# Performance work log

Measured on AMD Instinct MI355X. Metric: run time of the kernel, lower is better.

## Reference

```python
import jax, jax.numpy as jnp
import numpy as np

N = 50000      # nodes
E = 800000     # edges per meta-path
P = 3          # meta-paths
IN = 128       # in_size
H = 8          # heads
D = 32         # out_size per head
EMB = 128      # embedding_dim


def setup_inputs() -> dict:
    key = jax.random.key(0)
    ks = jax.random.split(key, 7)
    h = jax.random.normal(ks[0], (N, IN), jnp.float32)
    edge_index = jax.random.randint(ks[1], (P, 2, E), 0, N, dtype=jnp.int32)
    fc_w = jax.random.normal(ks[2], (P, IN, H * D), jnp.float32) * 0.05
    attn_l = jax.random.normal(ks[3], (P, H, D), jnp.float32) * 0.1
    attn_r = jax.random.normal(ks[4], (P, H, D), jnp.float32) * 0.1
    sem_w = jax.random.normal(ks[5], (P * H * D, EMB), jnp.float32) * 0.05
    sem_b = jnp.zeros((EMB,), jnp.float32)
    return {"h": h, "edge_index": edge_index, "fc_w": fc_w,
            "attn_l": attn_l, "attn_r": attn_r, "sem_w": sem_w, "sem_b": sem_b}


def _gat(h, W, al, ar, src, dst):
    # DGL GATConv (no bias/residual), eval mode (no dropout)
    feat = (h @ W).reshape(N, H, D)                      # (N,H,D)
    el = jnp.einsum('nhd,hd->nh', feat, al)              # (N,H)
    er = jnp.einsum('nhd,hd->nh', feat, ar)
    e = jax.nn.leaky_relu(el[src] + er[dst], negative_slope=0.2)  # (E,H)
    # edge softmax over incoming edges of each dst node
    m = jax.ops.segment_max(e, dst, num_segments=N)      # (N,H); -inf only for empty segs (never indexed)
    ex = jnp.exp(e - m[dst])
    den = jax.ops.segment_sum(ex, dst, num_segments=N)   # (N,H)
    a = ex / den[dst]                                    # (E,H)
    msg = feat[src] * a[..., None]                       # (E,H,D) gather + weight
    out = jax.ops.segment_sum(msg, dst, num_segments=N)  # (N,H,D) scatter-add
    return jax.nn.elu(out).reshape(N, H * D)             # flatten(1)


def reference(h, edge_index, fc_w, attn_l, attn_r, sem_w, sem_b):
    src = edge_index[:, 0]  # (P,E)
    dst = edge_index[:, 1]
    # run one GATConv per meta-path, vectorized over the meta-path axis
    z = jax.vmap(_gat, in_axes=(None, 0, 0, 0, 0, 0))(h, fc_w, attn_l, attn_r, src, dst)  # (P,N,H*D)
    z = jnp.transpose(z, (1, 0, 2)).reshape(N, P * H * D)  # stack(dim=1) then reshape [N,-1]
    return z @ sem_w + sem_b                                # SemanticAttention.project2
```

## Files before the change

kernel.cpp:

```cpp
#include <hip/hip_runtime.h>
#include <hip/hip_bf16.h>

#define N_NODES 50000
#define N_EDGES 800000
#define NPATH 3
#define NBKT 196
#define NBKT3 (NPATH * NBKT)
#define NCHUNKBLK 256
#define CHUNK 9375
#define LDS_STRIDE 260

typedef __attribute__((ext_vector_type(8))) short short8;
typedef __attribute__((ext_vector_type(4))) float v4f;

__device__ __forceinline__ short f2bf(float v, float* back) {
  unsigned u = __float_as_uint(v);
  unsigned r = (u + 0x7FFFu + ((u >> 16) & 1u)) >> 16;
  *back = __uint_as_float(r << 16);
  return (short)r;
}

__global__ __launch_bounds__(256) void blk_count_kernel(
    const int* __restrict__ ei, int* __restrict__ cntmat) {
  __shared__ int lcnt[NBKT3];
  const int t = threadIdx.x, blk = blockIdx.x;
  for (int j = t; j < NBKT3; j += 256) lcnt[j] = 0;
  __syncthreads();
  const int lo = blk * CHUNK, hi = lo + CHUNK;
  for (int idx = lo + t; idx < hi; idx += 256) {
    int p = idx / N_EDGES, e = idx - p * N_EDGES;
    int d = ei[p * 2 * N_EDGES + N_EDGES + e];
    atomicAdd(&lcnt[p * NBKT + (d >> 8)], 1);
  }
  __syncthreads();
  for (int j = t; j < NBKT3; j += 256) cntmat[blk * NBKT3 + j] = lcnt[j];
}

__global__ __launch_bounds__(256) void col_scan_kernel(
    const int* __restrict__ cntmat, int* __restrict__ pos, int* __restrict__ btot) {
  __shared__ int tmp[256];
  const int b = blockIdx.x, t = threadIdx.x;
  int v = cntmat[t * NBKT3 + b];
  tmp[t] = v;
  __syncthreads();
  for (int ofs = 1; ofs < 256; ofs <<= 1) {
    int x = (t >= ofs) ? tmp[t - ofs] : 0;
    __syncthreads();
    tmp[t] += x;
    __syncthreads();
  }
  pos[b * 256 + t] = tmp[t] - v;
  if (t == 255) btot[b] = tmp[255];
}

__global__ __launch_bounds__(1024) void bucket_scan_kernel(
    const int* __restrict__ btot, int* __restrict__ boff) {
  __shared__ int tmp[1024];
  const int t = threadIdx.x;
  int v = (t < NBKT3) ? btot[t] : 0;
  tmp[t] = v;
  __syncthreads();
  for (int ofs = 1; ofs < 1024; ofs <<= 1) {
    int x = (t >= ofs) ? tmp[t - ofs] : 0;
    __syncthreads();
    tmp[t] += x;
    __syncthreads();
  }
  if (t < NBKT3) boff[t] = tmp[t] - v;
}

__global__ __launch_bounds__(256) void scatter_det_kernel(
    const int* __restrict__ ei, const int* __restrict__ boff,
    const int* __restrict__ pos, int2* __restrict__ ebuf) {
  __shared__ int cursor[NBKT3];
  const int t = threadIdx.x, blk = blockIdx.x;
  for (int j = t; j < NBKT3; j += 256)
    cursor[j] = boff[j] + pos[j * 256 + blk];
  __syncthreads();
  const int lo = blk * CHUNK, hi = lo + CHUNK;
  for (int idx = lo + t; idx < hi; idx += 256) {
    int p = idx / N_EDGES, e = idx - p * N_EDGES;
    int s = ei[p * 2 * N_EDGES + e];
    int d = ei[p * 2 * N_EDGES + N_EDGES + e];
    int ps = atomicAdd(&cursor[p * NBKT + (d >> 8)], 1);
    ebuf[ps] = make_int2(s, d);
  }
}

__global__ __launch_bounds__(256) void bucket_csr_kernel(
    const int2* __restrict__ ebuf, const int* __restrict__ boff,
    const int* __restrict__ btot,
    int* __restrict__ off3, int* __restrict__ deg3, int* __restrict__ csr_src) {
  __shared__ int cnt[256], excl[256], cur[256];
  const int b = blockIdx.x;
  const int t = threadIdx.x;
  const int p = b / NBKT;
  const int node_base = (b - p * NBKT) * 256;
  const int start = boff[b];
  const int ecount = btot[b];

  cnt[t] = 0;
  __syncthreads();
  for (int i = t; i < ecount; i += 256)
    atomicAdd(&cnt[ebuf[start + i].y & 255], 1);
  __syncthreads();

  int v = cnt[t];
  excl[t] = v;
  __syncthreads();
  for (int ofs = 1; ofs < 256; ofs <<= 1) {
    int x = (t >= ofs) ? excl[t - ofs] : 0;
    __syncthreads();
    excl[t] += x;
    __syncthreads();
  }
  int my_excl = excl[t] - v;
  cur[t] = my_excl;
  const int node = node_base + t;
  if (node < N_NODES) {
    off3[p * N_NODES + node] = start + my_excl;
    deg3[p * N_NODES + node] = v;
  }
  __syncthreads();

  for (int i = t; i < ecount; i += 256) {
    int2 e = ebuf[start + i];
    int pos2 = atomicAdd(&cur[e.y & 255], 1);
    csr_src[start + pos2] = e.x;
  }
}

__global__ __launch_bounds__(256) void prep_kernel(
    const float* __restrict__ fc_w, const float* __restrict__ attn_l,
    const float* __restrict__ attn_r, const float* __restrict__ sem_w,
    __hip_bfloat16* __restrict__ Wf_hi, __hip_bfloat16* __restrict__ Wf_lo,
    __hip_bfloat16* __restrict__ Bs_hi, __hip_bfloat16* __restrict__ Bs_lo) {
  const int p = blockIdx.x / 33;
  const int unit = blockIdx.x % 33;
  const int t = threadIdx.x;
  if (unit < 17) {
    const float* W = fc_w + (size_t)p * 128 * 256;
    int idx = unit * 256 + t;
    int lane = idx & 63;
    int tmp = idx >> 6;
    int nt = tmp % 17, kc = tmp / 17;
    int l15 = lane & 15, quad = lane >> 4;
    __hip_bfloat16* oh = Wf_hi + (size_t)p * 34816;
    __hip_bfloat16* ol = Wf_lo + (size_t)p * 34816;
    for (int j = 0; j < 8; j++) {
      int k = kc * 32 + quad * 8 + j;
      float v;
      if (nt < 16) {
        v = W[k * 256 + nt * 16 + l15];
      } else {
        int h8 = l15 & 7;
        const float* av = ((l15 < 8) ? attn_l : attn_r) + (size_t)p * 256 + h8 * 32;
        v = 0.f;
        for (int dd = 0; dd < 32; dd++)
          v = fmaf(W[k * 256 + h8 * 32 + dd], av[dd], v);
      }
      float back, back2;
      short hb = f2bf(v, &back);
      short lb = f2bf(v - back, &back2);
      ((short*)oh)[(tmp * 64 + lane) * 8 + j] = hb;
      ((short*)ol)[(tmp * 64 + lane) * 8 + j] = lb;
    }
  } else {
    const float* Ws = sem_w + (size_t)p * 256 * 128;
    int idx = (unit - 17) * 256 + t;
    int lane = idx & 63;
    int tmp = idx >> 6;
    int nt = tmp & 7, kc = tmp >> 3;
    int l15 = lane & 15, quad = lane >> 4;
    __hip_bfloat16* oh = Bs_hi + (size_t)p * 32768;
    __hip_bfloat16* ol = Bs_lo + (size_t)p * 32768;
    for (int j = 0; j < 8; j++) {
      int k = kc * 32 + quad * 8 + j;
      float v = Ws[k * 128 + nt * 16 + l15];
      float back, back2;
      short hb = f2bf(v, &back);
      short lb = f2bf(v - back, &back2);
      ((short*)oh)[(tmp * 64 + lane) * 8 + j] = hb;
      ((short*)ol)[(tmp * 64 + lane) * 8 + j] = lb;
    }
  }
}

__global__ __launch_bounds__(64) void feat_mfma_kernel(
    const float* __restrict__ h,
    const __hip_bfloat16* __restrict__ Wf_hi_all,
    const __hip_bfloat16* __restrict__ Wf_lo_all,
    __hip_bfloat16* __restrict__ feat3, float* __restrict__ el3,
    float* __restrict__ er3) {
  const int p = blockIdx.y;
  const __hip_bfloat16* Wf_hi = Wf_hi_all + (size_t)p * 34816;
  const __hip_bfloat16* Wf_lo = Wf_lo_all + (size_t)p * 34816;
  __hip_bfloat16* feat = feat3 + (size_t)p * N_NODES * 256;
  float* el = el3 + (size_t)p * N_NODES * 8;
  float* er = er3 + (size_t)p * N_NODES * 8;

  const int lane = threadIdx.x;
  const int l15 = lane & 15, quad = lane >> 4;
  const int m0 = blockIdx.x * 16;
  const int mrow = m0 + l15;

  v4f acc[17];
#pragma unroll
  for (int nt = 0; nt < 17; nt++) acc[nt] = {0.f, 0.f, 0.f, 0.f};

#pragma unroll
  for (int kc = 0; kc < 4; kc++) {
    const float* hrow = h + (size_t)mrow * 128 + kc * 32 + quad * 8;
    float4 fa = *(const float4*)hrow;
    float4 fb = *(const float4*)(hrow + 4);
    float fv[8] = {fa.x, fa.y, fa.z, fa.w, fb.x, fb.y, fb.z, fb.w};
    short8 ahi, alo;
#pragma unroll
    for (int q = 0; q < 8; q++) {
      float back, back2;
      ahi[q] = f2bf(fv[q], &back);
      alo[q] = f2bf(fv[q] - back, &back2);
    }
#pragma unroll
    for (int nt = 0; nt < 17; nt++) {
      const int o = ((kc * 17 + nt) * 64 + lane) * 8;
      short8 bhi = *(const short8*)(Wf_hi + o);
      short8 blo = *(const short8*)(Wf_lo + o);
      acc[nt] = __builtin_amdgcn_mfma_f32_16x16x32_bf16(ahi, bhi, acc[nt], 0, 0, 0);
      acc[nt] = __builtin_amdgcn_mfma_f32_16x16x32_bf16(ahi, blo, acc[nt], 0, 0, 0);
      acc[nt] = __builtin_amdgcn_mfma_f32_16x16x32_bf16(alo, bhi, acc[nt], 0, 0, 0);
    }
  }

#pragma unroll
  for (int nt = 0; nt < 16; nt++)
#pragma unroll
    for (int r = 0; r < 4; r++) {
      int m = m0 + quad * 4 + r;
      feat[(size_t)m * 256 + nt * 16 + l15] = __float2bfloat16(acc[nt][r]);
    }
#pragma unroll
  for (int r = 0; r < 4; r++) {
    int m = m0 + quad * 4 + r;
    float v = acc[16][r];
    if (l15 < 8) el[m * 8 + l15] = v;
    else         er[m * 8 + (l15 - 8)] = v;
  }
}

__global__ __launch_bounds__(512) void agg_sem_kernel(
    const int* __restrict__ csr_src, const int* __restrict__ off,
    const int* __restrict__ deg,
    const float* __restrict__ el, const float* __restrict__ er,
    const __hip_bfloat16* __restrict__ feat,
    const __hip_bfloat16* __restrict__ Bs_hi, const __hip_bfloat16* __restrict__ Bs_lo,
    const float* __restrict__ bias, float* __restrict__ out, int mode) {
  __shared__ float Arow[16 * LDS_STRIDE];
  const int t = threadIdx.x;
  const int w = t >> 6, lane = t & 63;
  const int hh = lane >> 3;
  const int node_base = blockIdx.x * 16;
  const ushort* fp = (const ushort*)feat;

#pragma unroll
  for (int i = 0; i < 2; i++) {
    const int node = node_base + 2 * w + i;
    const int n = deg[node];
    const int* lst = csr_src + off[node];
    const float erh = er[node * 8 + hh];

    float aN0 = 0.f, aN1 = 0.f, aN2 = 0.f, aN3 = 0.f, aD = 0.f;
    int j = 0;
    for (; j + 4 <= n; j += 4) {
      int s0 = lst[j], s1 = lst[j + 1], s2 = lst[j + 2], s3 = lst[j + 3];
      float x0 = el[s0 * 8 + hh] + erh;
      float x1 = el[s1 * 8 + hh] + erh;
      float x2 = el[s2 * 8 + hh] + erh;
      float x3 = el[s3 * 8 + hh] + erh;
      ushort4 f0 = *(const ushort4*)(fp + (size_t)s0 * 256 + lane * 4);
      ushort4 f1 = *(const ushort4*)(fp + (size_t)s1 * 256 + lane * 4);
      ushort4 f2 = *(const ushort4*)(fp + (size_t)s2 * 256 + lane * 4);
      ushort4 f3 = *(const ushort4*)(fp + (size_t)s3 * 256 + lane * 4);
      x0 = x0 > 0.f ? x0 : 0.2f * x0;  float e0 = __expf(x0);
      x1 = x1 > 0.f ? x1 : 0.2f * x1;  float e1 = __expf(x1);
      x2 = x2 > 0.f ? x2 : 0.2f * x2;  float e2 = __expf(x2);
      x3 = x3 > 0.f ? x3 : 0.2f * x3;  float e3 = __expf(x3);
      aD += e0 + e1 + e2 + e3;
      aN0 = fmaf(e0, __uint_as_float((unsigned)f0.x << 16), aN0);
      aN1 = fmaf(e0, __uint_as_float((unsigned)f0.y << 16), aN1);
      aN2 = fmaf(e0, __uint_as_float((unsigned)f0.z << 16), aN2);
      aN3 = fmaf(e0, __uint_as_float((unsigned)f0.w << 16), aN3);
      aN0 = fmaf(e1, __uint_as_float((unsigned)f1.x << 16), aN0);
      aN1 = fmaf(e1, __uint_as_float((unsigned)f1.y << 16), aN1);
      aN2 = fmaf(e1, __uint_as_float((unsigned)f1.z << 16), aN2);
      aN3 = fmaf(e1, __uint_as_float((unsigned)f1.w << 16), aN3);
      aN0 = fmaf(e2, __uint_as_float((unsigned)f2.x << 16), aN0);
      aN1 = fmaf(e2, __uint_as_float((unsigned)f2.y << 16), aN1);
      aN2 = fmaf(e2, __uint_as_float((unsigned)f2.z << 16), aN2);
      aN3 = fmaf(e2, __uint_as_float((unsigned)f2.w << 16), aN3);
      aN0 = fmaf(e3, __uint_as_float((unsigned)f3.x << 16), aN0);
      aN1 = fmaf(e3, __uint_as_float((unsigned)f3.y << 16), aN1);
      aN2 = fmaf(e3, __uint_as_float((unsigned)f3.z << 16), aN2);
      aN3 = fmaf(e3, __uint_as_float((unsigned)f3.w << 16), aN3);
    }
    for (; j < n; j++) {
      int s = lst[j];
      float x = el[s * 8 + hh] + erh;
      ushort4 f0 = *(const ushort4*)(fp + (size_t)s * 256 + lane * 4);
      x = x > 0.f ? x : 0.2f * x;
      float e0 = __expf(x);
      aD += e0;
      aN0 = fmaf(e0, __uint_as_float((unsigned)f0.x << 16), aN0);
      aN1 = fmaf(e0, __uint_as_float((unsigned)f0.y << 16), aN1);
      aN2 = fmaf(e0, __uint_as_float((unsigned)f0.z << 16), aN2);
      aN3 = fmaf(e0, __uint_as_float((unsigned)f0.w << 16), aN3);
    }

    float inv = (n > 0) ? 1.f / aD : 0.f;
    float r0 = aN0 * inv, r1 = aN1 * inv, r2 = aN2 * inv, r3 = aN3 * inv;
    r0 = r0 > 0.f ? r0 : (__expf(r0) - 1.f);
    r1 = r1 > 0.f ? r1 : (__expf(r1) - 1.f);
    r2 = r2 > 0.f ? r2 : (__expf(r2) - 1.f);
    r3 = r3 > 0.f ? r3 : (__expf(r3) - 1.f);
    *(float4*)&Arow[(2 * w + i) * LDS_STRIDE + lane * 4] =
        make_float4(r0, r1, r2, r3);
  }
  __syncthreads();

  const int nt = w;
  const int l15 = lane & 15, quad = lane >> 4;
  v4f acc = {0.f, 0.f, 0.f, 0.f};
#pragma unroll
  for (int kc = 0; kc < 8; kc++) {
    const float* ap = &Arow[l15 * LDS_STRIDE + kc * 32 + quad * 8];
    float4 a0 = *(const float4*)ap;
    float4 a1 = *(const float4*)(ap + 4);
    float fv[8] = {a0.x, a0.y, a0.z, a0.w, a1.x, a1.y, a1.z, a1.w};
    short8 ahi, alo;
#pragma unroll
    for (int q = 0; q < 8; q++) {
      float back, back2;
      ahi[q] = f2bf(fv[q], &back);
      alo[q] = f2bf(fv[q] - back, &back2);
    }
    const int o = ((kc * 8 + nt) * 64 + lane) * 8;
    short8 bhi = *(const short8*)(Bs_hi + o);
    short8 blo = *(const short8*)(Bs_lo + o);
    acc = __builtin_amdgcn_mfma_f32_16x16x32_bf16(ahi, bhi, acc, 0, 0, 0);
    acc = __builtin_amdgcn_mfma_f32_16x16x32_bf16(ahi, blo, acc, 0, 0, 0);
    acc = __builtin_amdgcn_mfma_f32_16x16x32_bf16(alo, bhi, acc, 0, 0, 0);
  }

#pragma unroll
  for (int r = 0; r < 4; r++) {
    int m = node_base + quad * 4 + r;
    size_t o = (size_t)m * 128 + nt * 16 + l15;
    float v = acc[r];
    if (mode == 0) v += bias[nt * 16 + l15];
    else           v += out[o];
    out[o] = v;
  }
}

extern "C" void kernel_launch(void* const* d_in, const int* in_sizes, int n_in,
                              void* d_out, int out_size, void* d_ws, size_t ws_size,
                              hipStream_t stream) {
  const float* h      = (const float*)d_in[0];
  const int*   ei     = (const int*)d_in[1];
  const float* fc_w   = (const float*)d_in[2];
  const float* attn_l = (const float*)d_in[3];
  const float* attn_r = (const float*)d_in[4];
  const float* sem_w  = (const float*)d_in[5];
  const float* sem_b  = (const float*)d_in[6];
  float* out = (float*)d_out;

  char* ws = (char*)d_ws;
  __hip_bfloat16* feat3 = (__hip_bfloat16*)ws;
  float* el3     = (float*)(ws + 76800000);
  float* er3     = (float*)(ws + 81600000);
  int*   csr_src = (int*)(ws + 86400000);
  int2*  ebuf    = (int2*)(ws + 96000000);
  int*   deg3    = (int*)(ws + 115200000);
  int*   off3    = (int*)(ws + 115800000);
  int*   cntmat  = (int*)(ws + 116400000);
  int*   posm    = (int*)(ws + 117050000);
  int*   btot    = (int*)(ws + 117700000);
  int*   boff    = (int*)(ws + 117710000);
  __hip_bfloat16* Wf_hi = (__hip_bfloat16*)(ws + 117800000);
  __hip_bfloat16* Wf_lo = (__hip_bfloat16*)(ws + 118050000);
  __hip_bfloat16* Bs_hi = (__hip_bfloat16*)(ws + 118300000);
  __hip_bfloat16* Bs_lo = (__hip_bfloat16*)(ws + 118550000);

  blk_count_kernel<<<NCHUNKBLK, 256, 0, stream>>>(ei, cntmat);
  col_scan_kernel<<<NBKT3, 256, 0, stream>>>(cntmat, posm, btot);
  bucket_scan_kernel<<<1, 1024, 0, stream>>>(btot, boff);
  scatter_det_kernel<<<NCHUNKBLK, 256, 0, stream>>>(ei, boff, posm, ebuf);
  bucket_csr_kernel<<<NBKT3, 256, 0, stream>>>(ebuf, boff, btot, off3, deg3, csr_src);
  prep_kernel<<<NPATH * 33, 256, 0, stream>>>(fc_w, attn_l, attn_r, sem_w,
                                              Wf_hi, Wf_lo, Bs_hi, Bs_lo);

  feat_mfma_kernel<<<dim3(N_NODES / 16, NPATH), 64, 0, stream>>>(
      h, Wf_hi, Wf_lo, feat3, el3, er3);

  for (int p = 0; p < NPATH; p++) {
    agg_sem_kernel<<<N_NODES / 16, 512, 0, stream>>>(
        csr_src, off3 + p * N_NODES, deg3 + p * N_NODES,
        el3 + (size_t)p * N_NODES * 8, er3 + (size_t)p * N_NODES * 8,
        feat3 + (size_t)p * N_NODES * 256,
        Bs_hi + (size_t)p * 32768, Bs_lo + (size_t)p * 32768,
        sem_b, out, p);
  }
}
```

Baseline: 492.1 us.

## Double row tile in feature GEMM and interleave two-node edge aggregation

```diff
diff --git a/kernel.cpp b/kernel.cpp
--- a/kernel.cpp
+++ b/kernel.cpp
@@ -201,34 +201,48 @@
 
   const int lane = threadIdx.x;
   const int l15 = lane & 15, quad = lane >> 4;
-  const int m0 = blockIdx.x * 16;
-  const int mrow = m0 + l15;
-
-  v4f acc[17];
-#pragma unroll
-  for (int nt = 0; nt < 17; nt++) acc[nt] = {0.f, 0.f, 0.f, 0.f};
+  const int m0 = blockIdx.x * 32;
+  const bool okB = (m0 + 16) < N_NODES;
+  const int mrowA = m0 + l15;
+  const int mrowB = okB ? (m0 + 16 + l15) : mrowA;
+
+  v4f acc0[17], acc1[17];
+#pragma unroll
+  for (int nt = 0; nt < 17; nt++) {
+    acc0[nt] = {0.f, 0.f, 0.f, 0.f};
+    acc1[nt] = {0.f, 0.f, 0.f, 0.f};
+  }
 
 #pragma unroll
   for (int kc = 0; kc < 4; kc++) {
-    const float* hrow = h + (size_t)mrow * 128 + kc * 32 + quad * 8;
-    float4 fa = *(const float4*)hrow;
-    float4 fb = *(const float4*)(hrow + 4);
-    float fv[8] = {fa.x, fa.y, fa.z, fa.w, fb.x, fb.y, fb.z, fb.w};
-    short8 ahi, alo;
+    const float* hrowA = h + (size_t)mrowA * 128 + kc * 32 + quad * 8;
+    const float* hrowB = h + (size_t)mrowB * 128 + kc * 32 + quad * 8;
+    float4 a0 = *(const float4*)hrowA;
+    float4 a1 = *(const float4*)(hrowA + 4);
+    float4 b0 = *(const float4*)hrowB;
+    float4 b1 = *(const float4*)(hrowB + 4);
+    float fvA[8] = {a0.x, a0.y, a0.z, a0.w, a1.x, a1.y, a1.z, a1.w};
+    float fvB[8] = {b0.x, b0.y, b0.z, b0.w, b1.x, b1.y, b1.z, b1.w};
+    short8 ahiA, aloA, ahiB, aloB;
 #pragma unroll
     for (int q = 0; q < 8; q++) {
       float back, back2;
-      ahi[q] = f2bf(fv[q], &back);
-      alo[q] = f2bf(fv[q] - back, &back2);
+      ahiA[q] = f2bf(fvA[q], &back);
+      aloA[q] = f2bf(fvA[q] - back, &back2);
+      ahiB[q] = f2bf(fvB[q], &back);
+      aloB[q] = f2bf(fvB[q] - back, &back2);
     }
 #pragma unroll
     for (int nt = 0; nt < 17; nt++) {
       const int o = ((kc * 17 + nt) * 64 + lane) * 8;
       short8 bhi = *(const short8*)(Wf_hi + o);
       short8 blo = *(const short8*)(Wf_lo + o);
-      acc[nt] = __builtin_amdgcn_mfma_f32_16x16x32_bf16(ahi, bhi, acc[nt], 0, 0, 0);
-      acc[nt] = __builtin_amdgcn_mfma_f32_16x16x32_bf16(ahi, blo, acc[nt], 0, 0, 0);
-      acc[nt] = __builtin_amdgcn_mfma_f32_16x16x32_bf16(alo, bhi, acc[nt], 0, 0, 0);
+      acc0[nt] = __builtin_amdgcn_mfma_f32_16x16x32_bf16(ahiA, bhi, acc0[nt], 0, 0, 0);
+      acc0[nt] = __builtin_amdgcn_mfma_f32_16x16x32_bf16(ahiA, blo, acc0[nt], 0, 0, 0);
+      acc0[nt] = __builtin_amdgcn_mfma_f32_16x16x32_bf16(aloA, bhi, acc0[nt], 0, 0, 0);
+      acc1[nt] = __builtin_amdgcn_mfma_f32_16x16x32_bf16(ahiB, bhi, acc1[nt], 0, 0, 0);
+      acc1[nt] = __builtin_amdgcn_mfma_f32_16x16x32_bf16(ahiB, blo, acc1[nt], 0, 0, 0);
+      acc1[nt] = __builtin_amdgcn_mfma_f32_16x16x32_bf16(aloB, bhi, acc1[nt], 0, 0, 0);
     }
   }
 
@@ -237,15 +251,74 @@
 #pragma unroll
     for (int r = 0; r < 4; r++) {
       int m = m0 + quad * 4 + r;
-      feat[(size_t)m * 256 + nt * 16 + l15] = __float2bfloat16(acc[nt][r]);
+      feat[(size_t)m * 256 + nt * 16 + l15] = __float2bfloat16(acc0[nt][r]);
+      if (okB)
+        feat[(size_t)(m + 16) * 256 + nt * 16 + l15] = __float2bfloat16(acc1[nt][r]);
     }
 #pragma unroll
   for (int r = 0; r < 4; r++) {
     int m = m0 + quad * 4 + r;
-    float v = acc[16][r];
-    if (l15 < 8) el[m * 8 + l15] = v;
-    else         er[m * 8 + (l15 - 8)] = v;
-  }
+    float v0 = acc0[16][r];
+    if (l15 < 8) el[m * 8 + l15] = v0;
+    else         er[m * 8 + (l15 - 8)] = v0;
+    if (okB) {
+      float v1 = acc1[16][r];
+      if (l15 < 8) el[(m + 16) * 8 + l15] = v1;
+      else         er[(m + 16) * 8 + (l15 - 8)] = v1;
+    }
+  }
+}
+
+__device__ __forceinline__ void edge4(
+    const int* __restrict__ lst, int j, const float* __restrict__ el,
+    float erh, const ushort* __restrict__ fp, int lane, int hh,
+    float& aD, float& aN0, float& aN1, float& aN2, float& aN3) {
+  int s0 = lst[j], s1 = lst[j + 1], s2 = lst[j + 2], s3 = lst[j + 3];
+  float x0 = el[s0 * 8 + hh] + erh;
+  float x1 = el[s1 * 8 + hh] + erh;
+  float x2 = el[s2 * 8 + hh] + erh;
+  float x3 = el[s3 * 8 + hh] + erh;
+  ushort4 f0 = *(const ushort4*)(fp + (size_t)s0 * 256 + lane * 4);
+  ushort4 f1 = *(const ushort4*)(fp + (size_t)s1 * 256 + lane * 4);
+  ushort4 f2 = *(const ushort4*)(fp + (size_t)s2 * 256 + lane * 4);
+  ushort4 f3 = *(const ushort4*)(fp + (size_t)s3 * 256 + lane * 4);
+  x0 = x0 > 0.f ? x0 : 0.2f * x0;  float e0 = __expf(x0);
+  x1 = x1 > 0.f ? x1 : 0.2f * x1;  float e1 = __expf(x1);
+  x2 = x2 > 0.f ? x2 : 0.2f * x2;  float e2 = __expf(x2);
+  x3 = x3 > 0.f ? x3 : 0.2f * x3;  float e3 = __expf(x3);
+  aD += e0 + e1 + e2 + e3;
+  aN0 = fmaf(e0, __uint_as_float((unsigned)f0.x << 16), aN0);
+  aN1 = fmaf(e0, __uint_as_float((unsigned)f0.y << 16), aN1);
+  aN2 = fmaf(e0, __uint_as_float((unsigned)f0.z << 16), aN2);
+  aN3 = fmaf(e0, __uint_as_float((unsigned)f0.w << 16), aN3);
+  aN0 = fmaf(e1, __uint_as_float((unsigned)f1.x << 16), aN0);
+  aN1 = fmaf(e1, __uint_as_float((unsigned)f1.y << 16), aN1);
+  aN2 = fmaf(e1, __uint_as_float((unsigned)f1.z << 16), aN2);
+  aN3 = fmaf(e1, __uint_as_float((unsigned)f1.w << 16), aN3);
+  aN0 = fmaf(e2, __uint_as_float((unsigned)f2.x << 16), aN0);
+  aN1 = fmaf(e2, __uint_as_float((unsigned)f2.y << 16), aN1);
+  aN2 = fmaf(e2, __uint_as_float((unsigned)f2.z << 16), aN2);
+  aN3 = fmaf(e2, __uint_as_float((unsigned)f2.w << 16), aN3);
+  aN0 = fmaf(e3, __uint_as_float((unsigned)f3.x << 16), aN0);
+  aN1 = fmaf(e3, __uint_as_float((unsigned)f3.y << 16), aN1);
+  aN2 = fmaf(e3, __uint_as_float((unsigned)f3.z << 16), aN2);
+  aN3 = fmaf(e3, __uint_as_float((unsigned)f3.w << 16), aN3);
+}
+
+__device__ __forceinline__ void edge1(
+    const int* __restrict__ lst, int j, const float* __restrict__ el,
+    float erh, const ushort* __restrict__ fp, int lane, int hh,
+    float& aD, float& aN0, float& aN1, float& aN2, float& aN3) {
+  int s = lst[j];
+  float x = el[s * 8 + hh] + erh;
+  ushort4 f0 = *(const ushort4*)(fp + (size_t)s * 256 + lane * 4);
+  x = x > 0.f ? x : 0.2f * x;
+  float e0 = __expf(x);
+  aD += e0;
+  aN0 = fmaf(e0, __uint_as_float((unsigned)f0.x << 16), aN0);
+  aN1 = fmaf(e0, __uint_as_float((unsigned)f0.y << 16), aN1);
+  aN2 = fmaf(e0, __uint_as_float((unsigned)f0.z << 16), aN2);
+  aN3 = fmaf(e0, __uint_as_float((unsigned)f0.w << 16), aN3);
 }
 
 __global__ __launch_bounds__(512) void agg_sem_kernel(
@@ -262,68 +335,47 @@
   const int node_base = blockIdx.x * 16;
   const ushort* fp = (const ushort*)feat;
 
-#pragma unroll
-  for (int i = 0; i < 2; i++) {
-    const int node = node_base + 2 * w + i;
-    const int n = deg[node];
-    const int* lst = csr_src + off[node];
-    const float erh = er[node * 8 + hh];
-
-    float aN0 = 0.f, aN1 = 0.f, aN2 = 0.f, aN3 = 0.f, aD = 0.f;
-    int j = 0;
-    for (; j + 4 <= n; j += 4) {
-      int s0 = lst[j], s1 = lst[j + 1], s2 = lst[j + 2], s3 = lst[j + 3];
-      float x0 = el[s0 * 8 + hh] + erh;
-      float x1 = el[s1 * 8 + hh] + erh;
-      float x2 = el[s2 * 8 + hh] + erh;
-      float x3 = el[s3 * 8 + hh] + erh;
-      ushort4 f0 = *(const ushort4*)(fp + (size_t)s0 * 256 + lane * 4);
-      ushort4 f1 = *(const ushort4*)(fp + (size_t)s1 * 256 + lane * 4);
-      ushort4 f2 = *(const ushort4*)(fp + (size_t)s2 * 256 + lane * 4);
-      ushort4 f3 = *(const ushort4*)(fp + (size_t)s3 * 256 + lane * 4);
-      x0 = x0 > 0.f ? x0 : 0.2f * x0;  float e0 = __expf(x0);
-      x1 = x1 > 0.f ? x1 : 0.2f * x1;  float e1 = __expf(x1);
-      x2 = x2 > 0.f ? x2 : 0.2f * x2;  float e2 = __expf(x2);
-      x3 = x3 > 0.f ? x3 : 0.2f * x3;  float e3 = __expf(x3);
-      aD += e0 + e1 + e2 + e3;
-      aN0 = fmaf(e0, __uint_as_float((unsigned)f0.x << 16), aN0);
-      aN1 = fmaf(e0, __uint_as_float((unsigned)f0.y << 16), aN1);
-      aN2 = fmaf(e0, __uint_as_float((unsigned)f0.z << 16), aN2);
-      aN3 = fmaf(e0, __uint_as_float((unsigned)f0.w << 16), aN3);
-      aN0 = fmaf(e1, __uint_as_float((unsigned)f1.x << 16), aN0);
-      aN1 = fmaf(e1, __uint_as_float((unsigned)f1.y << 16), aN1);
-      aN2 = fmaf(e1, __uint_as_float((unsigned)f1.z << 16), aN2);
-      aN3 = fmaf(e1, __uint_as_float((unsigned)f1.w << 16), aN3);
-      aN0 = fmaf(e2, __uint_as_float((unsigned)f2.x << 16), aN0);
-      aN1 = fmaf(e2, __uint_as_float((unsigned)f2.y << 16), aN1);
-      aN2 = fmaf(e2, __uint_as_float((unsigned)f2.z << 16), aN2);
-      aN3 = fmaf(e2, __uint_as_float((unsigned)f2.w << 16), aN3);
-      aN0 = fmaf(e3, __uint_as_float((unsigned)f3.x << 16), aN0);
-      aN1 = fmaf(e3, __uint_as_float((unsigned)f3.y << 16), aN1);
-      aN2 = fmaf(e3, __uint_as_float((unsigned)f3.z << 16), aN2);
-      aN3 = fmaf(e3, __uint_as_float((unsigned)f3.w << 16), aN3);
-    }
-    for (; j < n; j++) {
-      int s = lst[j];
-      float x = el[s * 8 + hh] + erh;
-      ushort4 f0 = *(const ushort4*)(fp + (size_t)s * 256 + lane * 4);
-      x = x > 0.f ? x : 0.2f * x;
-      float e0 = __expf(x);
-      aD += e0;
-      aN0 = fmaf(e0, __uint_as_float((unsigned)f0.x << 16), aN0);
-      aN1 = fmaf(e0, __uint_as_float((unsigned)f0.y << 16), aN1);
-      aN2 = fmaf(e0, __uint_as_float((unsigned)f0.z << 16), aN2);
-      aN3 = fmaf(e0, __uint_as_float((unsigned)f0.w << 16), aN3);
-    }
-
-    float inv = (n > 0) ? 1.f / aD : 0.f;
-    float r0 = aN0 * inv, r1 = aN1 * inv, r2 = aN2 * inv, r3 = aN3 * inv;
+  const int node0 = node_base + 2 * w;
+  const int node1 = node0 + 1;
+  const int n0 = deg[node0], n1 = deg[node1];
+  const int* lst0 = csr_src + off[node0];
+  const int* lst1 = csr_src + off[node1];
+  const float erh0 = er[node0 * 8 + hh];
+  const float erh1 = er[node1 * 8 + hh];
+
+  float p0 = 0.f, p1 = 0.f, p2 = 0.f, p3 = 0.f, pD = 0.f;
+  float q0 = 0.f, q1 = 0.f, q2 = 0.f, q3 = 0.f, qD = 0.f;
+
+  const int nmin = min(n0, n1);
+  int j = 0;
+  for (; j + 4 <= nmin; j += 4) {
+    edge4(lst0, j, el, erh0, fp, lane, hh, pD, p0, p1, p2, p3);
+    edge4(lst1, j, el, erh1, fp, lane, hh, qD, q0, q1, q2, q3);
+  }
+  int ja = j;
+  for (; ja + 4 <= n0; ja += 4) edge4(lst0, ja, el, erh0, fp, lane, hh, pD, p0, p1, p2, p3);
+  for (; ja < n0; ja++)         edge1(lst0, ja, el, erh0, fp, lane, hh, pD, p0, p1, p2, p3);
+  int jb = j;
+  for (; jb + 4 <= n1; jb += 4) edge4(lst1, jb, el, erh1, fp, lane, hh, qD, q0, q1, q2, q3);
+  for (; jb < n1; jb++)         edge1(lst1, jb, el, erh1, fp, lane, hh, qD, q0, q1, q2, q3);
+
+  {
+    float inv = (n0 > 0) ? 1.f / pD : 0.f;
+    float r0 = p0 * inv, r1 = p1 * inv, r2 = p2 * inv, r3 = p3 * inv;
     r0 = r0 > 0.f ? r0 : (__expf(r0) - 1.f);
     r1 = r1 > 0.f ? r1 : (__expf(r1) - 1.f);
     r2 = r2 > 0.f ? r2 : (__expf(r2) - 1.f);
     r3 = r3 > 0.f ? r3 : (__expf(r3) - 1.f);
-    *(float4*)&Arow[(2 * w + i) * LDS_STRIDE + lane * 4] =
-        make_float4(r0, r1, r2, r3);
+    *(float4*)&Arow[(2 * w) * LDS_STRIDE + lane * 4] = make_float4(r0, r1, r2, r3);
+  }
+  {
+    float inv = (n1 > 0) ? 1.f / qD : 0.f;
+    float r0 = q0 * inv, r1 = q1 * inv, r2 = q2 * inv, r3 = q3 * inv;
+    r0 = r0 > 0.f ? r0 : (__expf(r0) - 1.f);
+    r1 = r1 > 0.f ? r1 : (__expf(r1) - 1.f);
+    r2 = r2 > 0.f ? r2 : (__expf(r2) - 1.f);
+    r3 = r3 > 0.f ? r3 : (__expf(r3) - 1.f);
+    *(float4*)&Arow[(2 * w + 1) * LDS_STRIDE + lane * 4] = make_float4(r0, r1, r2, r3);
   }
   __syncthreads();
 
@@ -399,7 +451,7 @@
   prep_kernel<<<NPATH * 33, 256, 0, stream>>>(fc_w, attn_l, attn_r, sem_w,
                                               Wf_hi, Wf_lo, Bs_hi, Bs_lo);
 
-  feat_mfma_kernel<<<dim3(N_NODES / 16, NPATH), 64, 0, stream>>>(
+  feat_mfma_kernel<<<dim3((N_NODES + 31) / 32, NPATH), 64, 0, stream>>>(
       h, Wf_hi, Wf_lo, feat3, el3, er3);
 
   for (int p = 0; p < NPATH; p++) {
```

Measured after the change: 535.4 us. 1.09x slower.
